# Kernel tuning notes

Measured on AMD Instinct MI355X. Metric: run time of the kernel, lower is better.

## Reference

```python
import jax, jax.numpy as jnp
import numpy as np

N = 262144      # nodes per graph
NC = 65536      # common nodes
D = 256         # feature_dim


def setup_inputs() -> dict:
    key = jax.random.key(0)
    ks = jax.random.split(key, 12)
    h_prop = jax.random.normal(ks[0], (N, D), dtype=jnp.float32)
    h_context = jax.random.normal(ks[1], (N, D), dtype=jnp.float32)
    h_orig = jax.random.normal(ks[2], (NC, D), dtype=jnp.float32)
    # unique indices (torch scatter-assign semantics are only well-defined without dups)
    idx_prop = jnp.sort(jax.random.permutation(ks[3], N)[:NC]).astype(jnp.int64)
    idx_ctx = jnp.sort(jax.random.permutation(ks[4], N)[:NC]).astype(jnp.int64)
    # parameters (xavier-ish scale)
    s = 1.0 / np.sqrt(D)
    w_orig = jax.random.normal(ks[5], (D, D), dtype=jnp.float32) * s
    w_prop = jax.random.normal(ks[6], (D, D), dtype=jnp.float32) * s
    w_ctx = jax.random.normal(ks[7], (D, D), dtype=jnp.float32) * s
    W_fuse = jax.random.normal(ks[8], (D, 3 * D), dtype=jnp.float32) * (1.0 / np.sqrt(3 * D))  # torch Linear weight (out,in)
    b_fuse = jnp.zeros((D,), dtype=jnp.float32)
    bias = jax.random.uniform(ks[9], (D,), dtype=jnp.float32, minval=-s, maxval=s)
    return {
        "h_prop": h_prop, "h_context": h_context,
        "h_original_common_nodes": h_orig,
        "w_orig": w_orig, "w_prop": w_prop, "w_ctx": w_ctx,
        "W_fuse": W_fuse, "b_fuse": b_fuse, "bias": bias,
        "common_node_indices_in_prop": idx_prop,
        "common_node_indices_in_context": idx_ctx,
    }


def reference(h_prop, h_context, h_original_common_nodes,
              w_orig, w_prop, w_ctx, W_fuse, b_fuse, bias,
              common_node_indices_in_prop, common_node_indices_in_context):
    # gather common rows + three small GEMMs  [NC, D]
    t_orig = h_original_common_nodes @ w_orig
    t_prop = h_prop[common_node_indices_in_prop] @ w_prop
    t_ctx = h_context[common_node_indices_in_context] @ w_ctx
    # concat-linear-tanh-bias  [NC, D]
    fused = jnp.concatenate([t_orig, t_prop, t_ctx], axis=1) @ W_fuse.T + b_fuse
    fused = jnp.tanh(fused) + bias
    # scatter update into clones of the full tables
    h_prop_updated = h_prop.at[common_node_indices_in_prop].set(fused)
    h_context_updated = h_context.at[common_node_indices_in_context].set(fused)
    return (h_prop_updated, h_context_updated)
```

## Files before the change

kernel.cpp:

```cpp
#include <hip/hip_runtime.h>
#include <hip/hip_bf16.h>
#include <math.h>

#define NN 262144
#define NCC 65536

typedef __bf16 bf16x8 __attribute__((ext_vector_type(8)));
typedef float f32x4 __attribute__((ext_vector_type(4)));

__global__ __launch_bounds__(256) void k_setup(const float* __restrict__ w_orig,
                                               const float* __restrict__ w_prop,
                                               const float* __restrict__ w_ctx,
                                               const float* __restrict__ W_fuse,
                                               __bf16* __restrict__ Mt,
                                               unsigned char* __restrict__ flags) {
    __shared__ float Wl[64 * 65];
    __shared__ float wl[64 * 65];
    int b = blockIdx.x;
    int t = threadIdx.x;
    if (b >= 48) {
        ((uint4*)flags)[(b - 48) * 256 + t] = make_uint4(0u, 0u, 0u, 0u);
        return;
    }
    int seg = b >> 4, rem = b & 15;
    int ot = rem >> 2, mt = rem & 3;
    const float* wseg = seg == 0 ? w_orig : (seg == 1 ? w_prop : w_ctx);
    int to = (t & 15) * 4, tm = (t >> 4) * 4;
    float acc[4][4] = {};
    for (int kc = 0; kc < 4; ++kc) {
        __syncthreads();
        for (int i = 0; i < 16; ++i) {
            int f = i * 256 + t;
            int row = f >> 6, col = f & 63;
            Wl[row * 65 + col] = W_fuse[(size_t)(ot * 64 + row) * 768 + seg * 256 + kc * 64 + col];
            wl[row * 65 + col] = wseg[(size_t)(mt * 64 + row) * 256 + kc * 64 + col];
        }
        __syncthreads();
        for (int k = 0; k < 64; ++k) {
            float wo[4], wm2[4];
#pragma unroll
            for (int i = 0; i < 4; ++i) wo[i] = Wl[(to + i) * 65 + k];
#pragma unroll
            for (int j = 0; j < 4; ++j) wm2[j] = wl[(tm + j) * 65 + k];
#pragma unroll
            for (int i = 0; i < 4; ++i)
#pragma unroll
                for (int j = 0; j < 4; ++j) acc[i][j] += wo[i] * wm2[j];
        }
    }
    for (int i = 0; i < 4; ++i)
        for (int j = 0; j < 4; ++j) {
            int o = ot * 64 + to + i;
            int g = seg * 256 + mt * 64 + tm + j;
            Mt[(size_t)o * 768 + g] = (__bf16)acc[i][j];
        }
}

__global__ void k_setflags(const int* __restrict__ idxp, const int* __restrict__ idxc,
                           unsigned char* fp, unsigned char* fc) {
    int j = blockIdx.x * blockDim.x + threadIdx.x;
    if (j < NCC) { fp[idxp[j]] = 1; fc[idxc[j]] = 1; }
}

__device__ inline bf16x8 cvt8(f32x4 a, f32x4 b) {
    bf16x8 w;
    w[0] = (__bf16)a[0]; w[1] = (__bf16)a[1]; w[2] = (__bf16)a[2]; w[3] = (__bf16)a[3];
    w[4] = (__bf16)b[0]; w[5] = (__bf16)b[1]; w[6] = (__bf16)b[2]; w[7] = (__bf16)b[3];
    return w;
}

__global__ __launch_bounds__(512, 4) void k_gemm(const float* __restrict__ hp,
                                                 const float* __restrict__ hc,
                                                 const float* __restrict__ horig,
                                                 const __bf16* __restrict__ Mt,
                                                 const float* __restrict__ bfuse,
                                                 const float* __restrict__ bias,
                                                 const int* __restrict__ idxp,
                                                 const int* __restrict__ idxc,
                                                 float* __restrict__ out0,
                                                 float* __restrict__ out1) {
    __shared__ __bf16 Al[64 * 64];
    __shared__ __bf16 Bl[256 * 64];
    int t = threadIdx.x;
    int jbase = blockIdx.x * 64;
    int lane = t & 63, wid = t >> 6;
    int wm = wid >> 2, wn = wid & 3;
    int l15 = lane & 15, lq = lane >> 4;

    int ar = t >> 3, aslot = t & 7;
    int jr = jbase + ar;
    const float* rowp0 = horig + (size_t)jr * 256 + aslot * 8;
    const float* rowp1 = hp + (size_t)idxp[jr] * 256 + aslot * 8;
    const float* rowp2 = hc + (size_t)idxc[jr] * 256 + aslot * 8;

    int bo = t >> 1, bkp = t & 1;
    const __bf16* bsrc = Mt + (size_t)bo * 768 + bkp * 32;

    f32x4 acc[2][4] = {};

    f32x4 va0 = *(const f32x4*)(rowp0);
    f32x4 va1 = *(const f32x4*)(rowp0 + 4);
    bf16x8 vb[4];
#pragma unroll
    for (int i = 0; i < 4; ++i) vb[i] = *(const bf16x8*)(bsrc + i * 8);

#pragma unroll
    for (int c = 0; c < 12; ++c) {
        __syncthreads();
        *(bf16x8*)&Al[ar * 64 + ((aslot ^ (ar & 7)) << 3)] = cvt8(va0, va1);
#pragma unroll
        for (int i = 0; i < 4; ++i) {
            int slot = bkp * 4 + i;
            *(bf16x8*)&Bl[bo * 64 + ((slot ^ (bo & 7)) << 3)] = vb[i];
        }
        if (c < 11) {
            int cn = c + 1;
            int seg = cn >> 2, ko = (cn & 3) * 64;
            const float* s = (seg == 0 ? rowp0 : (seg == 1 ? rowp1 : rowp2)) + ko;
            va0 = *(const f32x4*)(s);
            va1 = *(const f32x4*)(s + 4);
#pragma unroll
            for (int i = 0; i < 4; ++i) vb[i] = *(const bf16x8*)(bsrc + cn * 64 + i * 8);
        }
        __syncthreads();
#pragma unroll
        for (int ks = 0; ks < 2; ++ks) {
            bf16x8 af[2], bfr[4];
            int kslot = ks * 4 + lq;
#pragma unroll
            for (int mi = 0; mi < 2; ++mi) {
                int r = wm * 32 + mi * 16 + l15;
                af[mi] = *(const bf16x8*)&Al[r * 64 + ((kslot ^ (r & 7)) << 3)];
            }
#pragma unroll
            for (int ni = 0; ni < 4; ++ni) {
                int o = wn * 64 + ni * 16 + l15;
                bfr[ni] = *(const bf16x8*)&Bl[o * 64 + ((kslot ^ (o & 7)) << 3)];
            }
#pragma unroll
            for (int mi = 0; mi < 2; ++mi)
#pragma unroll
                for (int ni = 0; ni < 4; ++ni)
                    acc[mi][ni] = __builtin_amdgcn_mfma_f32_16x16x32_bf16(af[mi], bfr[ni], acc[mi][ni], 0, 0, 0);
        }
    }

    float bfv[4], biv[4];
#pragma unroll
    for (int ni = 0; ni < 4; ++ni) {
        int o = wn * 64 + ni * 16 + l15;
        bfv[ni] = bfuse[o];
        biv[ni] = bias[o];
    }
#pragma unroll
    for (int mi = 0; mi < 2; ++mi) {
#pragma unroll
        for (int rr = 0; rr < 4; ++rr) {
            int j = jbase + wm * 32 + mi * 16 + lq * 4 + rr;
            int gp = idxp[j];
            int gc = idxc[j];
#pragma unroll
            for (int ni = 0; ni < 4; ++ni) {
                int o = wn * 64 + ni * 16 + l15;
                float v = tanhf(acc[mi][ni][rr] + bfv[ni]) + biv[ni];
                out0[(size_t)gp * 256 + o] = v;
                out1[(size_t)gc * 256 + o] = v;
            }
        }
    }
}

__global__ __launch_bounds__(256) void k_copy(const float* __restrict__ hp,
                                              const float* __restrict__ hc,
                                              const unsigned char* __restrict__ fp,
                                              const unsigned char* __restrict__ fc,
                                              float* __restrict__ out0,
                                              float* __restrict__ out1) {
    int tid = blockIdx.x * 256 + threadIdx.x;
    const int stride = 4096 * 256;
#pragma unroll
    for (int it = 0; it < 32; ++it) {
        int gid = it * stride + tid;
        int row = gid >> 6, slot = gid & 63;
        int tbl = row >= NN;
        int r = tbl ? row - NN : row;
        const unsigned char* F = tbl ? fc : fp;
        const float* S = tbl ? hc : hp;
        float* D = tbl ? out1 : out0;
        unsigned char f = F[r];
        const float* s = S + (size_t)(f ? 0 : r) * 256 + slot * 4;
        f32x4 v = *(const f32x4*)s;
        if (!f) *(f32x4*)(D + (size_t)r * 256 + slot * 4) = v;
    }
}

extern "C" void kernel_launch(void* const* d_in, const int* in_sizes, int n_in,
                              void* d_out, int out_size, void* d_ws, size_t ws_size,
                              hipStream_t stream) {
    const float* hp     = (const float*)d_in[0];
    const float* hc     = (const float*)d_in[1];
    const float* horig  = (const float*)d_in[2];
    const float* w_orig = (const float*)d_in[3];
    const float* w_prop = (const float*)d_in[4];
    const float* w_ctx  = (const float*)d_in[5];
    const float* W_fuse = (const float*)d_in[6];
    const float* bfuse  = (const float*)d_in[7];
    const float* bias   = (const float*)d_in[8];
    const int* idxp     = (const int*)d_in[9];
    const int* idxc     = (const int*)d_in[10];
    float* out0 = (float*)d_out;
    float* out1 = out0 + (size_t)NN * 256;

    char* ws = (char*)d_ws;
    __bf16* Mt = (__bf16*)ws;
    unsigned char* fp = (unsigned char*)(ws + 393216);
    unsigned char* fc = fp + NN;

    k_setup<<<176, 256, 0, stream>>>(w_orig, w_prop, w_ctx, W_fuse, Mt, fp);
    k_setflags<<<NCC / 256, 256, 0, stream>>>(idxp, idxc, fp, fc);
    k_gemm<<<NCC / 64, 512, 0, stream>>>(hp, hc, horig, Mt, bfuse, bias,
                                         idxp, idxc, out0, out1);
    k_copy<<<4096, 256, 0, stream>>>(hp, hc, fp, fc, out0, out1);
}
```

Before: 323.7 us.

## Stage GEMM epilogue through LDS for vector scatter stores; deepen prefetch and batch copy loads

The GEMM epilogue now writes tanh results into per-wave LDS scratch and then scatters them as 16-byte vector stores per row, replacing scalar strided stores. The A-operand global prefetch is pushed two chunks ahead using double registers. The copy kernel groups eight flag loads, then eight data loads, then eight stores, to raise memory-level parallelism. The aim is to cut uncoalesced store traffic and load latency, at the cost of more registers, extra LDS and another barrier.

New measurement: 324.9 us. Within noise of the previous version (+0.4%).

```diff
diff --git a/kernel.cpp b/kernel.cpp
--- a/kernel.cpp
+++ b/kernel.cpp
@@ -79,8 +79,9 @@
                                                  const int* __restrict__ idxc,
                                                  float* __restrict__ out0,
                                                  float* __restrict__ out1) {
-    __shared__ __bf16 Al[64 * 64];
-    __shared__ __bf16 Bl[256 * 64];
+    __shared__ char smem[40960];
+    __bf16* Al = (__bf16*)smem;
+    __bf16* Bl = (__bf16*)(smem + 8192);
     int t = threadIdx.x;
     int jbase = blockIdx.x * 64;
     int lane = t & 63, wid = t >> 6;
@@ -96,31 +97,37 @@
     int bo = t >> 1, bkp = t & 1;
     const __bf16* bsrc = Mt + (size_t)bo * 768 + bkp * 32;
 
+    f32x4 a0[2], a1[2];
+    bf16x8 vb[4];
+    {
+        a0[0] = *(const f32x4*)(rowp0);       a1[0] = *(const f32x4*)(rowp0 + 4);
+        a0[1] = *(const f32x4*)(rowp0 + 64);  a1[1] = *(const f32x4*)(rowp0 + 68);
+#pragma unroll
+        for (int i = 0; i < 4; ++i) vb[i] = *(const bf16x8*)(bsrc + i * 8);
+    }
+
     f32x4 acc[2][4] = {};
 
-    f32x4 va0 = *(const f32x4*)(rowp0);
-    f32x4 va1 = *(const f32x4*)(rowp0 + 4);
-    bf16x8 vb[4];
-#pragma unroll
-    for (int i = 0; i < 4; ++i) vb[i] = *(const bf16x8*)(bsrc + i * 8);
-
 #pragma unroll
     for (int c = 0; c < 12; ++c) {
-        __syncthreads();
-        *(bf16x8*)&Al[ar * 64 + ((aslot ^ (ar & 7)) << 3)] = cvt8(va0, va1);
+        int s = c & 1;
+        __syncthreads();
+        *(bf16x8*)&Al[ar * 64 + ((aslot ^ (ar & 7)) << 3)] = cvt8(a0[s], a1[s]);
 #pragma unroll
         for (int i = 0; i < 4; ++i) {
             int slot = bkp * 4 + i;
             *(bf16x8*)&Bl[bo * 64 + ((slot ^ (bo & 7)) << 3)] = vb[i];
         }
         if (c < 11) {
-            int cn = c + 1;
+#pragma unroll
+            for (int i = 0; i < 4; ++i) vb[i] = *(const bf16x8*)(bsrc + (c + 1) * 64 + i * 8);
+        }
+        if (c < 10) {
+            int cn = c + 2;
             int seg = cn >> 2, ko = (cn & 3) * 64;
-            const float* s = (seg == 0 ? rowp0 : (seg == 1 ? rowp1 : rowp2)) + ko;
-            va0 = *(const f32x4*)(s);
-            va1 = *(const f32x4*)(s + 4);
-#pragma unroll
-            for (int i = 0; i < 4; ++i) vb[i] = *(const bf16x8*)(bsrc + cn * 64 + i * 8);
+            const float* sp = (seg == 0 ? rowp0 : (seg == 1 ? rowp1 : rowp2)) + ko;
+            a0[s] = *(const f32x4*)(sp);
+            a1[s] = *(const f32x4*)(sp + 4);
         }
         __syncthreads();
 #pragma unroll
@@ -152,20 +159,25 @@
         bfv[ni] = bfuse[o];
         biv[ni] = bias[o];
     }
+    __syncthreads();
+    float* scr = (float*)(smem + 8192 + wid * 4096);
 #pragma unroll
     for (int mi = 0; mi < 2; ++mi) {
 #pragma unroll
-        for (int rr = 0; rr < 4; ++rr) {
-            int j = jbase + wm * 32 + mi * 16 + lq * 4 + rr;
-            int gp = idxp[j];
-            int gc = idxc[j];
-#pragma unroll
-            for (int ni = 0; ni < 4; ++ni) {
-                int o = wn * 64 + ni * 16 + l15;
+        for (int ni = 0; ni < 4; ++ni)
+#pragma unroll
+            for (int rr = 0; rr < 4; ++rr) {
                 float v = tanhf(acc[mi][ni][rr] + bfv[ni]) + biv[ni];
-                out0[(size_t)gp * 256 + o] = v;
-                out1[(size_t)gc * 256 + o] = v;
+                scr[(lq * 4 + rr) * 64 + ni * 16 + l15] = v;
             }
+#pragma unroll
+        for (int rnd = 0; rnd < 4; ++rnd) {
+            int rr2 = rnd * 4 + lq;
+            int j = jbase + wm * 32 + mi * 16 + rr2;
+            int gp = idxp[j], gc = idxc[j];
+            f32x4 v = *(const f32x4*)&scr[rr2 * 64 + l15 * 4];
+            *(f32x4*)(out0 + (size_t)gp * 256 + wn * 64 + l15 * 4) = v;
+            *(f32x4*)(out1 + (size_t)gc * 256 + wn * 64 + l15 * 4) = v;
         }
     }
 }
@@ -179,18 +191,35 @@
     int tid = blockIdx.x * 256 + threadIdx.x;
     const int stride = 4096 * 256;
 #pragma unroll
-    for (int it = 0; it < 32; ++it) {
-        int gid = it * stride + tid;
-        int row = gid >> 6, slot = gid & 63;
-        int tbl = row >= NN;
-        int r = tbl ? row - NN : row;
-        const unsigned char* F = tbl ? fc : fp;
-        const float* S = tbl ? hc : hp;
-        float* D = tbl ? out1 : out0;
-        unsigned char f = F[r];
-        const float* s = S + (size_t)(f ? 0 : r) * 256 + slot * 4;
-        f32x4 v = *(const f32x4*)s;
-        if (!f) *(f32x4*)(D + (size_t)r * 256 + slot * 4) = v;
+    for (int g = 0; g < 4; ++g) {
+        unsigned char fl[8];
+#pragma unroll
+        for (int i = 0; i < 8; ++i) {
+            int gid = (g * 8 + i) * stride + tid;
+            int row = gid >> 6;
+            int tbl = row >= NN;
+            int r = tbl ? row - NN : row;
+            fl[i] = (tbl ? fc : fp)[r];
+        }
+        f32x4 v[8];
+#pragma unroll
+        for (int i = 0; i < 8; ++i) {
+            int gid = (g * 8 + i) * stride + tid;
+            int row = gid >> 6, slot = gid & 63;
+            int tbl = row >= NN;
+            int r = tbl ? row - NN : row;
+            const float* S = tbl ? hc : hp;
+            v[i] = *(const f32x4*)(S + (size_t)(fl[i] ? 0 : r) * 256 + slot * 4);
+        }
+#pragma unroll
+        for (int i = 0; i < 8; ++i) {
+            int gid = (g * 8 + i) * stride + tid;
+            int row = gid >> 6, slot = gid & 63;
+            int tbl = row >= NN;
+            int r = tbl ? row - NN : row;
+            float* D = tbl ? out1 : out0;
+            if (!fl[i]) *(f32x4*)(D + (size_t)r * 256 + slot * 4) = v[i];
+        }
     }
 }
 
```
